# Kernel optimization log

Hardware: AMD Instinct MI355X
Metric: run time of the kernel (lower is better)

Reference implementation:

```python
import jax, jax.numpy as jnp
import numpy as np

M1, M2 = 16, 16  # Fourier modes per dim


def conv1x1(x, w, b):
    # x: [B,Ci,H,W], w: [Co,Ci], b: [Co]
    return jnp.einsum('bihw,oi->bohw', x, w) + b[None, :, None, None]


def fno_block(x, wr, wi, bw, bb):
    # x: [B,C,H,W]; wr/wi: [C,C,M1,M2]; bw: [C,C]; bb: [C]
    H, W = x.shape[-2], x.shape[-1]
    x_fft = jnp.fft.rfftn(x, axes=(-2, -1), norm='ortho')[:, :, :M1, :M2]
    w = (wr + 1j * wi).astype(jnp.complex64)
    out_fft = jnp.einsum('bikl,iokl->bokl', x_fft, w)
    # irfftn with s zero-pads truncated modes back to full spatial size
    x_spec = jnp.fft.irfftn(out_fft, s=(H, W), axes=(-2, -1), norm='ortho')
    return jax.nn.gelu(x_spec + conv1x1(x, bw, bb), approximate=False)


def setup_inputs() -> dict:
    key = jax.random.key(0)
    ks = jax.random.split(key, 8)
    B, in_c, H, W = 4, 3, 256, 256
    out_c, n_blocks, width = 4, 4, 32
    scale = 1.0 / (width * width)
    return {
        'x': jax.random.normal(ks[0], (B, in_c, H, W), jnp.float32),
        'lift_w': jax.random.normal(ks[1], (width, in_c), jnp.float32) * 0.1,
        'lift_b': jnp.zeros((width,), jnp.float32),
        'wr': jax.random.normal(ks[2], (out_c, n_blocks, width, width, M1, M2), jnp.float32) * scale,
        'wi': jax.random.normal(ks[3], (out_c, n_blocks, width, width, M1, M2), jnp.float32) * scale,
        'byp_w': jax.random.normal(ks[4], (out_c, n_blocks, width, width), jnp.float32) * 0.1,
        'byp_b': jnp.zeros((out_c, n_blocks, width), jnp.float32),
        'proj_w': jax.random.normal(ks[5], (1, width), jnp.float32) * 0.1,
        'proj_b': jnp.zeros((1,), jnp.float32),
    }


def reference(x, lift_w, lift_b, wr, wi, byp_w, byp_b, proj_w, proj_b):
    out_c, n_blocks = wr.shape[0], wr.shape[1]
    x0 = conv1x1(x, lift_w, lift_b)
    outputs = []
    for o in range(out_c):
        xb = x0
        for n in range(n_blocks):
            xb = fno_block(xb, wr[o, n], wi[o, n], byp_w[o, n], byp_b[o, n])
        outputs.append(conv1x1(xb, proj_w, proj_b))
    return jnp.concatenate(outputs, axis=1)
```

## Files before the change

### kernel.cpp

```cpp
#include <hip/hip_runtime.h>

#define NB 4
#define NC 32
#define NH 256
#define NW 256
#define NM 16
constexpr int NPIX = NH * NW;
constexpr int NP = NB * NC * NPIX;
constexpr int ZG = NB * NC * NM * NM * 2;

typedef short bf16x8 __attribute__((ext_vector_type(8)));
typedef float f32x4  __attribute__((ext_vector_type(4)));
typedef unsigned short u16;

#define MFMA16(a, b, c) __builtin_amdgcn_mfma_f32_16x16x32_bf16(a, b, c, 0, 0, 0)

__device__ __forceinline__ u16 f2bf(float f) {
    unsigned u = __float_as_uint(f);
    u += 0x7FFFu + ((u >> 16) & 1u);
    return (u16)(u >> 16);
}
__device__ __forceinline__ float bf2f(u16 h) {
    return __uint_as_float(((unsigned)h) << 16);
}

__device__ __forceinline__ float gelu_fast(float v) {
    const float ax = fabsf(v) * 0.70710678118654752f;
    const float t = __builtin_amdgcn_rcpf(1.0f + 0.3275911f * ax);
    const float y = t * (0.254829592f + t * (-0.284496736f + t * (1.421413741f +
                    t * (-1.453152027f + t * 1.061405429f))));
    const float e = __expf(-ax * ax);
    float er = 1.0f - y * e;
    er = copysignf(er, v);
    return 0.5f * v * (1.0f + er);
}

__global__ __launch_bounds__(256) void cw_prep(u16* __restrict__ cwhi, u16* __restrict__ cwlo) {
    const int id = blockIdx.x * 256 + threadIdx.x;
    const int nn = id >> 5, k = id & 31;
    const int m = ((k & 15) * nn) & 255;
    float s, c;
    sincospif((float)m * (2.0f / 256.0f), &s, &c);
    const float v = (k < 16) ? c : s;
    const u16 hi = f2bf(v);
    cwhi[id] = hi;
    cwlo[id] = f2bf(v - bf2f(hi));
}

__global__ __launch_bounds__(256) void eb_prep(u16* __restrict__ ebhi, u16* __restrict__ eblo) {
    const int id = blockIdx.x * 256 + threadIdx.x;
    const int row = id >> 8, w = id & 255;
    const int m = ((row & 15) * w) & 255;
    float s, c;
    sincospif((float)m * (2.0f / 256.0f), &s, &c);
    const float v = 0.0625f * ((row < 16) ? c : s);
    const u16 hi = f2bf(v);
    ebhi[id] = hi;
    eblo[id] = f2bf(v - bf2f(hi));
}

template<bool LIFT>
__global__ __launch_bounds__(512) void fwd_kernel(
    const float* __restrict__ src,
    const float* __restrict__ lift_w,
    const float* __restrict__ lift_b,
    const u16* __restrict__ ebhi,
    const u16* __restrict__ eblo,
    float* __restrict__ zred)
{
    __shared__ u16 Yhi[32 * 260], Ylo[32 * 260];
    __shared__ float P[32][33];

    const int tid = threadIdx.x;
    const int c  = blockIdx.x;
    const int gb = blockIdx.y;
    const int b  = gb & 3;
    const int wv = tid >> 6, lane = tid & 63;
    const int mrow = lane & 15, q = lane >> 4;

    float lw0 = 0.f, lw1 = 0.f, lw2 = 0.f, lb = 0.f;
    const float* sb;
    if (LIFT) {
        lw0 = lift_w[c * 3 + 0]; lw1 = lift_w[c * 3 + 1]; lw2 = lift_w[c * 3 + 2];
        lb = lift_b[c];
        sb = src + (size_t)b * 3 * NPIX;
    } else {
        sb = src + ((size_t)gb * NC + c) * NPIX;
    }

    f32x4 acc[2][2] = {};
    for (int ks = 0; ks < 8; ++ks) {
        bf16x8 bh[2], bl[2];
        #pragma unroll
        for (int nt = 0; nt < 2; ++nt) {
            const int off = (nt * 16 + mrow) * 256 + ks * 32 + q * 8;
            bh[nt] = *(const bf16x8*)(ebhi + off);
            bl[nt] = *(const bf16x8*)(eblo + off);
        }
        #pragma unroll
        for (int mt = 0; mt < 2; ++mt) {
            const int h = wv * 32 + mt * 16 + mrow;
            const float* xp = sb + (size_t)h * NW + ks * 32 + q * 8;
            float v[8];
            if (LIFT) {
                const float4 p0a = *(const float4*)(xp);
                const float4 p0b = *(const float4*)(xp + 4);
                const float4 p1a = *(const float4*)(xp + NPIX);
                const float4 p1b = *(const float4*)(xp + NPIX + 4);
                const float4 p2a = *(const float4*)(xp + 2 * NPIX);
                const float4 p2b = *(const float4*)(xp + 2 * NPIX + 4);
                v[0] = lw0 * p0a.x + lw1 * p1a.x + lw2 * p2a.x + lb;
                v[1] = lw0 * p0a.y + lw1 * p1a.y + lw2 * p2a.y + lb;
                v[2] = lw0 * p0a.z + lw1 * p1a.z + lw2 * p2a.z + lb;
                v[3] = lw0 * p0a.w + lw1 * p1a.w + lw2 * p2a.w + lb;
                v[4] = lw0 * p0b.x + lw1 * p1b.x + lw2 * p2b.x + lb;
                v[5] = lw0 * p0b.y + lw1 * p1b.y + lw2 * p2b.y + lb;
                v[6] = lw0 * p0b.z + lw1 * p1b.z + lw2 * p2b.z + lb;
                v[7] = lw0 * p0b.w + lw1 * p1b.w + lw2 * p2b.w + lb;
            } else {
                const float4 pa = *(const float4*)(xp);
                const float4 pb = *(const float4*)(xp + 4);
                v[0] = pa.x; v[1] = pa.y; v[2] = pa.z; v[3] = pa.w;
                v[4] = pb.x; v[5] = pb.y; v[6] = pb.z; v[7] = pb.w;
            }
            bf16x8 xh, xl;
            #pragma unroll
            for (int j = 0; j < 8; ++j) {
                const u16 hi = f2bf(v[j]);
                xh[j] = (short)hi;
                xl[j] = (short)f2bf(v[j] - bf2f(hi));
            }
            #pragma unroll
            for (int nt = 0; nt < 2; ++nt) {
                acc[mt][nt] = MFMA16(xh, bh[nt], acc[mt][nt]);
                acc[mt][nt] = MFMA16(xh, bl[nt], acc[mt][nt]);
                acc[mt][nt] = MFMA16(xl, bh[nt], acc[mt][nt]);
            }
        }
    }

    #pragma unroll
    for (int mt = 0; mt < 2; ++mt) {
        #pragma unroll
        for (int nt = 0; nt < 2; ++nt) {
            #pragma unroll
            for (int r = 0; r < 4; ++r) {
                const int h = wv * 32 + mt * 16 + q * 4 + r;
                const int combo = nt * 16 + mrow;
                const float val = acc[mt][nt][r];
                const u16 hi = f2bf(val);
                Yhi[combo * 260 + h] = hi;
                Ylo[combo * 260 + h] = f2bf(val - bf2f(hi));
            }
        }
    }
    __syncthreads();

    if (wv < 4) {
        const int mt2 = wv >> 1, nt2 = wv & 1;
        f32x4 p = {};
        for (int ks = 0; ks < 8; ++ks) {
            const int aoff = (mt2 * 16 + mrow) * 256 + ks * 32 + q * 8;
            const bf16x8 ah = *(const bf16x8*)(ebhi + aoff);
            const bf16x8 al = *(const bf16x8*)(eblo + aoff);
            const int boff = (nt2 * 16 + mrow) * 260 + ks * 32 + q * 8;
            const bf16x8 yh = *(const bf16x8*)(Yhi + boff);
            const bf16x8 yl = *(const bf16x8*)(Ylo + boff);
            p = MFMA16(ah, yh, p);
            p = MFMA16(ah, yl, p);
            p = MFMA16(al, yh, p);
        }
        #pragma unroll
        for (int r = 0; r < 4; ++r)
            P[mt2 * 16 + q * 4 + r][nt2 * 16 + mrow] = p[r];
    }
    __syncthreads();

    if (tid < 256) {
        const int k = tid >> 4, l = tid & 15;
        const float zr = P[k][l] - P[16 + k][16 + l];
        const float zi = -(P[k][16 + l] + P[16 + k][l]);
        const int idx = (gb * NC + c) * 256 + tid;
        zred[idx * 2 + 0] = zr;
        zred[idx * 2 + 1] = zi;
    }
}

__global__ __launch_bounds__(256) void mix_kernel(
    const float* __restrict__ zred,
    float* __restrict__ zmix,
    const float* __restrict__ wr,
    const float* __restrict__ wi,
    int o0, int n, int zgmul)
{
    __shared__ float ps[4][NB][64][2];
    const int tid = threadIdx.x;
    const int oc = blockIdx.x, mq = blockIdx.y, g = blockIdx.z;
    const int o = o0 + g, zg = zgmul * g;
    const int ichunk = tid >> 6, ml = tid & 63;
    const int mode = mq * 64 + ml;

    const float* wrb = wr + (size_t)(o * 4 + n) * NC * NC * 256;
    const float* wib = wi + (size_t)(o * 4 + n) * NC * NC * 256;

    float orr[NB] = {0.f, 0.f, 0.f, 0.f};
    float oii[NB] = {0.f, 0.f, 0.f, 0.f};

    #pragma unroll
    for (int ii = 0; ii < 8; ++ii) {
        const int i = ichunk * 8 + ii;
        const float wrv = wrb[(i * NC + oc) * 256 + mode];
        const float wiv = wib[(i * NC + oc) * 256 + mode];
        #pragma unroll
        for (int b = 0; b < NB; ++b) {
            const float2 z = *(const float2*)&zred[(((zg * NB + b) * NC + i) * 256 + mode) * 2];
            orr[b] += z.x * wrv - z.y * wiv;
            oii[b] += z.x * wiv + z.y * wrv;
        }
    }
    #pragma unroll
    for (int b = 0; b < NB; ++b) {
        ps[ichunk][b][ml][0] = orr[b];
        ps[ichunk][b][ml][1] = oii[b];
    }
    __syncthreads();

    const int b2 = tid >> 6, ml2 = tid & 63;
    float re = 0.f, im = 0.f;
    #pragma unroll
    for (int ic = 0; ic < 4; ++ic) {
        re += ps[ic][b2][ml2][0];
        im += ps[ic][b2][ml2][1];
    }
    const int oidx = ((g * NB + b2) * NC + oc) * 256 + mq * 64 + ml2;
    zmix[oidx * 2 + 0] = re;
    zmix[oidx * 2 + 1] = im;
}

template<bool LIFT, bool FINAL>
__global__ __launch_bounds__(256) void inv_kernel(
    const float* __restrict__ zmix,
    const float* __restrict__ src,
    const float* __restrict__ byp_w,
    const float* __restrict__ byp_b,
    const float* __restrict__ lift_w,
    const float* __restrict__ lift_b,
    const float* __restrict__ proj_w,
    const float* __restrict__ proj_b,
    const u16* __restrict__ cwhi,
    const u16* __restrict__ cwlo,
    float* __restrict__ dst,
    int o0, int n)
{
    __shared__ float2 tw[256];
    __shared__ u16 Thi[NC * 40], Tlo[NC * 40];
    __shared__ u16 Whi[NC * 40], Wlo[NC * 40];
    __shared__ float bbl[NC];
    __shared__ float bweffs[NC * 3];

    const int tid = threadIdx.x;
    const int h = blockIdx.x;
    const int gb = blockIdx.y;
    const int g = gb >> 2, b = gb & 3;
    const int o = o0 + g;

    {
        float s, cs;
        sincospif((float)tid * (2.0f / 256.0f), &s, &cs);
        tw[tid] = make_float2(cs, s);
    }

    const float* bwp = byp_w + (size_t)(o * 4 + n) * NC * NC;
    const float* bbp = byp_b + (o * 4 + n) * NC;

    if (LIFT) {
        if (tid < 96) {
            const int oc = tid / 3, j = tid % 3;
            float s = 0.f;
            for (int ic = 0; ic < NC; ++ic) s += bwp[oc * NC + ic] * lift_w[ic * 3 + j];
            bweffs[oc * 3 + j] = s;
        } else if (tid < 128) {
            const int oc = tid - 96;
            float s = bbp[oc];
            for (int ic = 0; ic < NC; ++ic) s += bwp[oc * NC + ic] * lift_b[ic];
            bbl[oc] = s;
        }
    } else {
        if (tid < NC) bbl[tid] = bbp[tid];
    }
    __syncthreads();

    for (int idx = tid; idx < NC * NC; idx += 256) {
        const int c = idx >> 5, ic = idx & 31;
        float v;
        if (LIFT) v = (ic < 3) ? bweffs[c * 3 + ic] : 0.f;
        else      v = bwp[idx];
        const u16 hi = f2bf(v);
        Whi[c * 40 + ic] = hi;
        Wlo[c * 40 + ic] = f2bf(v - bf2f(hi));
    }

    #pragma unroll
    for (int rep = 0; rep < 2; ++rep) {
        const int it = rep * 256 + tid;
        const int c = it >> 4, l = it & 15;
        const float sl = (l == 0 ? 1.0f : 2.0f) / 256.0f;
        const float* zp = zmix + ((size_t)(gb * NC + c) * 256 + l) * 2;
        float tr = 0.f, ti = 0.f;
        int m = 0;
        #pragma unroll
        for (int k = 0; k < NM; ++k) {
            const float2 z = *(const float2*)(zp + k * 32);
            const float2 t = tw[m];
            tr += z.x * t.x - z.y * t.y;
            ti += z.x * t.y + z.y * t.x;
            m = (m + h) & 255;
        }
        tr *= sl; ti *= sl;
        if (l == 0) tr += bbl[c];
        const u16 rh = f2bf(tr);
        Thi[c * 40 + l] = rh;
        Tlo[c * 40 + l] = f2bf(tr - bf2f(rh));
        const float nti_ = -ti;
        const u16 ih = f2bf(nti_);
        Thi[c * 40 + 16 + l] = ih;
        Tlo[c * 40 + 16 + l] = f2bf(nti_ - bf2f(ih));
    }
    __syncthreads();

    const int lane = tid & 63, wv = tid >> 6;
    const int mrow = lane & 15, q = lane >> 4;

    bf16x8 aThi[2], aTlo[2], aWhi[2], aWlo[2];
    #pragma unroll
    for (int mt = 0; mt < 2; ++mt) {
        const int ro = (mt * 16 + mrow) * 40 + 8 * q;
        aThi[mt] = *(const bf16x8*)&Thi[ro];
        aTlo[mt] = *(const bf16x8*)&Tlo[ro];
        aWhi[mt] = *(const bf16x8*)&Whi[ro];
        aWlo[mt] = *(const bf16x8*)&Wlo[ro];
    }

    float pwv[8];
    float pb = 0.f;
    if (FINAL) {
        #pragma unroll
        for (int mt = 0; mt < 2; ++mt)
            #pragma unroll
            for (int i = 0; i < 4; ++i)
                pwv[mt * 4 + i] = proj_w[mt * 16 + q * 4 + i];
        pb = proj_b[0];
    }

    const float* xb = src + (LIFT ? (size_t)b * 3 * NPIX : (size_t)gb * NC * NPIX) + h * NW;
    const int KIC = LIFT ? 3 : NC;

    for (int nti = 0; nti < 4; ++nti) {
        const int nt = wv * 4 + nti;
        const int ncol = nt * 16 + mrow;

        const bf16x8 cwh = *(const bf16x8*)(cwhi + ncol * 32 + 8 * q);
        const bf16x8 cwl = *(const bf16x8*)(cwlo + ncol * 32 + 8 * q);

        bf16x8 xh, xl;
        #pragma unroll
        for (int j = 0; j < 8; ++j) {
            const int k = 8 * q + j;
            const float v = (k < KIC) ? xb[(size_t)k * NPIX + ncol] : 0.f;
            const u16 hi = f2bf(v);
            xh[j] = (short)hi;
            xl[j] = (short)f2bf(v - bf2f(hi));
        }

        float fpart = 0.f;
        #pragma unroll
        for (int mt = 0; mt < 2; ++mt) {
            f32x4 acc = {0.f, 0.f, 0.f, 0.f};
            acc = MFMA16(aThi[mt], cwh, acc);
            acc = MFMA16(aThi[mt], cwl, acc);
            acc = MFMA16(aTlo[mt], cwh, acc);
            acc = MFMA16(aWhi[mt], xh, acc);
            acc = MFMA16(aWhi[mt], xl, acc);
            acc = MFMA16(aWlo[mt], xh, acc);
            if (FINAL) {
                #pragma unroll
                for (int i = 0; i < 4; ++i)
                    fpart += gelu_fast(acc[i]) * pwv[mt * 4 + i];
            } else {
                #pragma unroll
                for (int i = 0; i < 4; ++i) {
                    const int c = mt * 16 + q * 4 + i;
                    dst[((size_t)gb * NC + c) * NPIX + h * NW + ncol] = gelu_fast(acc[i]);
                }
            }
        }
        if (FINAL) {
            fpart += __shfl_xor(fpart, 16);
            fpart += __shfl_xor(fpart, 32);
            if (q == 0) {
                dst[(((size_t)b * 4 + o) * NH + h) * NW + nt * 16 + mrow] = fpart + pb;
            }
        }
    }
}

extern "C" void kernel_launch(void* const* d_in, const int* in_sizes, int n_in,
                              void* d_out, int out_size, void* d_ws, size_t ws_size,
                              hipStream_t stream)
{
    const float* x      = (const float*)d_in[0];
    const float* lift_w = (const float*)d_in[1];
    const float* lift_b = (const float*)d_in[2];
    const float* wr     = (const float*)d_in[3];
    const float* wi     = (const float*)d_in[4];
    const float* byp_w  = (const float*)d_in[5];
    const float* byp_b  = (const float*)d_in[6];
    const float* proj_w = (const float*)d_in[7];
    const float* proj_b = (const float*)d_in[8];
    float* out = (float*)d_out;
    float* ws  = (float*)d_ws;

    u16* cwhi = (u16*)ws;
    u16* cwlo = cwhi + 8192;
    u16* ebhi = cwlo + 8192;
    u16* eblo = ebhi + 8192;
    float* base = ws + 16384;

    int G = 4;
    while (G > 1) {
        const size_t need = (16384 + (size_t)2 * G * NP + (size_t)2 * G * ZG) * sizeof(float);
        if (need <= ws_size) break;
        G >>= 1;
    }

    float* bufA = base;
    float* bufB = bufA + (size_t)G * NP;
    float* zred = bufB + (size_t)G * NP;
    float* zmix = zred + (size_t)G * ZG;

    cw_prep<<<32, 256, 0, stream>>>(cwhi, cwlo);
    eb_prep<<<32, 256, 0, stream>>>(ebhi, eblo);

    for (int o0 = 0; o0 < 4; o0 += G) {
        const float* rd = nullptr;
        float* wrbuf = bufA;
        for (int n = 0; n < 4; ++n) {
            const bool lift = (n == 0);
            const bool fin  = (n == 3);
            const float* src = lift ? x : rd;

            if (lift) {
                fwd_kernel<true><<<dim3(NC, NB), 512, 0, stream>>>(src, lift_w, lift_b, ebhi, eblo, zred);
            } else {
                fwd_kernel<false><<<dim3(NC, G * NB), 512, 0, stream>>>(src, lift_w, lift_b, ebhi, eblo, zred);
            }

            mix_kernel<<<dim3(NC, 4, G), 256, 0, stream>>>(zred, zmix, wr, wi, o0, n, lift ? 0 : 1);

            dim3 igrid(NH, G * NB);
            if (fin) {
                inv_kernel<false, true><<<igrid, 256, 0, stream>>>(
                    zmix, src, byp_w, byp_b, lift_w, lift_b, proj_w, proj_b, cwhi, cwlo, out, o0, n);
            } else if (lift) {
                inv_kernel<true, false><<<igrid, 256, 0, stream>>>(
                    zmix, src, byp_w, byp_b, lift_w, lift_b, proj_w, proj_b, cwhi, cwlo, wrbuf, o0, n);
            } else {
                inv_kernel<false, false><<<igrid, 256, 0, stream>>>(
                    zmix, src, byp_w, byp_b, lift_w, lift_b, proj_w, proj_b, cwhi, cwlo, wrbuf, o0, n);
            }
            rd = wrbuf;
            wrbuf = (wrbuf == bufA) ? bufB : bufA;
        }
    }
}
```

Baseline: 547.7 us.

## Split forward DFT into two kernels for more blocks, shrink mix blocks, cap G at 2

Splits the forward truncated DFT into two kernels. The first does the W-direction transform over 64-row slabs, four blocks per channel, and writes the bf16 hi/lo intermediate to global memory. The second does the H-direction reduction. This gives four times as many blocks for the expensive first stage, at the cost of an extra launch and a global round-trip of the intermediate. It also halves mix_kernel block size to double its grid, merges the two table-prep kernels into one, and lowers the maximum group size G from 4 to 2, which doubles the number of outer passes.

```diff
diff --git a/kernel.cpp b/kernel.cpp
--- a/kernel.cpp
+++ b/kernel.cpp
@@ -35,48 +35,53 @@
     return 0.5f * v * (1.0f + er);
 }
 
-__global__ __launch_bounds__(256) void cw_prep(u16* __restrict__ cwhi, u16* __restrict__ cwlo) {
+__global__ __launch_bounds__(256) void tab_prep(
+    u16* __restrict__ cwhi, u16* __restrict__ cwlo,
+    u16* __restrict__ ebhi, u16* __restrict__ eblo)
+{
     const int id = blockIdx.x * 256 + threadIdx.x;
-    const int nn = id >> 5, k = id & 31;
-    const int m = ((k & 15) * nn) & 255;
-    float s, c;
-    sincospif((float)m * (2.0f / 256.0f), &s, &c);
-    const float v = (k < 16) ? c : s;
-    const u16 hi = f2bf(v);
-    cwhi[id] = hi;
-    cwlo[id] = f2bf(v - bf2f(hi));
-}
-
-__global__ __launch_bounds__(256) void eb_prep(u16* __restrict__ ebhi, u16* __restrict__ eblo) {
-    const int id = blockIdx.x * 256 + threadIdx.x;
-    const int row = id >> 8, w = id & 255;
-    const int m = ((row & 15) * w) & 255;
-    float s, c;
-    sincospif((float)m * (2.0f / 256.0f), &s, &c);
-    const float v = 0.0625f * ((row < 16) ? c : s);
-    const u16 hi = f2bf(v);
-    ebhi[id] = hi;
-    eblo[id] = f2bf(v - bf2f(hi));
+    if (id < 8192) {
+        const int nn = id >> 5, k = id & 31;
+        const int m = ((k & 15) * nn) & 255;
+        float s, c;
+        sincospif((float)m * (2.0f / 256.0f), &s, &c);
+        const float v = (k < 16) ? c : s;
+        const u16 hi = f2bf(v);
+        cwhi[id] = hi;
+        cwlo[id] = f2bf(v - bf2f(hi));
+    } else {
+        const int id2 = id - 8192;
+        const int row = id2 >> 8, w = id2 & 255;
+        const int m = ((row & 15) * w) & 255;
+        float s, c;
+        sincospif((float)m * (2.0f / 256.0f), &s, &c);
+        const float v = 0.0625f * ((row < 16) ? c : s);
+        const u16 hi = f2bf(v);
+        ebhi[id2] = hi;
+        eblo[id2] = f2bf(v - bf2f(hi));
+    }
 }
 
 template<bool LIFT>
-__global__ __launch_bounds__(512) void fwd_kernel(
+__global__ __launch_bounds__(256) void fwd_s1(
     const float* __restrict__ src,
     const float* __restrict__ lift_w,
     const float* __restrict__ lift_b,
     const u16* __restrict__ ebhi,
     const u16* __restrict__ eblo,
-    float* __restrict__ zred)
+    u16* __restrict__ yhi,
+    u16* __restrict__ ylo)
 {
-    __shared__ u16 Yhi[32 * 260], Ylo[32 * 260];
-    __shared__ float P[32][33];
+    __shared__ u16 TrHi[64][34], TrLo[64][34];
 
     const int tid = threadIdx.x;
     const int c  = blockIdx.x;
     const int gb = blockIdx.y;
+    const int hq = blockIdx.z;
     const int b  = gb & 3;
     const int wv = tid >> 6, lane = tid & 63;
     const int mrow = lane & 15, q = lane >> 4;
+    const int hbase = hq * 64 + wv * 16;
 
     float lw0 = 0.f, lw1 = 0.f, lw2 = 0.f, lb = 0.f;
     const float* sb;
@@ -88,7 +93,7 @@
         sb = src + ((size_t)gb * NC + c) * NPIX;
     }
 
-    f32x4 acc[2][2] = {};
+    f32x4 acc[2] = {};
     for (int ks = 0; ks < 8; ++ks) {
         bf16x8 bh[2], bl[2];
         #pragma unroll
@@ -97,108 +102,126 @@
             bh[nt] = *(const bf16x8*)(ebhi + off);
             bl[nt] = *(const bf16x8*)(eblo + off);
         }
-        #pragma unroll
-        for (int mt = 0; mt < 2; ++mt) {
-            const int h = wv * 32 + mt * 16 + mrow;
-            const float* xp = sb + (size_t)h * NW + ks * 32 + q * 8;
-            float v[8];
-            if (LIFT) {
-                const float4 p0a = *(const float4*)(xp);
-                const float4 p0b = *(const float4*)(xp + 4);
-                const float4 p1a = *(const float4*)(xp + NPIX);
-                const float4 p1b = *(const float4*)(xp + NPIX + 4);
-                const float4 p2a = *(const float4*)(xp + 2 * NPIX);
-                const float4 p2b = *(const float4*)(xp + 2 * NPIX + 4);
-                v[0] = lw0 * p0a.x + lw1 * p1a.x + lw2 * p2a.x + lb;
-                v[1] = lw0 * p0a.y + lw1 * p1a.y + lw2 * p2a.y + lb;
-                v[2] = lw0 * p0a.z + lw1 * p1a.z + lw2 * p2a.z + lb;
-                v[3] = lw0 * p0a.w + lw1 * p1a.w + lw2 * p2a.w + lb;
-                v[4] = lw0 * p0b.x + lw1 * p1b.x + lw2 * p2b.x + lb;
-                v[5] = lw0 * p0b.y + lw1 * p1b.y + lw2 * p2b.y + lb;
-                v[6] = lw0 * p0b.z + lw1 * p1b.z + lw2 * p2b.z + lb;
-                v[7] = lw0 * p0b.w + lw1 * p1b.w + lw2 * p2b.w + lb;
-            } else {
-                const float4 pa = *(const float4*)(xp);
-                const float4 pb = *(const float4*)(xp + 4);
-                v[0] = pa.x; v[1] = pa.y; v[2] = pa.z; v[3] = pa.w;
-                v[4] = pb.x; v[5] = pb.y; v[6] = pb.z; v[7] = pb.w;
-            }
-            bf16x8 xh, xl;
-            #pragma unroll
-            for (int j = 0; j < 8; ++j) {
-                const u16 hi = f2bf(v[j]);
-                xh[j] = (short)hi;
-                xl[j] = (short)f2bf(v[j] - bf2f(hi));
-            }
-            #pragma unroll
-            for (int nt = 0; nt < 2; ++nt) {
-                acc[mt][nt] = MFMA16(xh, bh[nt], acc[mt][nt]);
-                acc[mt][nt] = MFMA16(xh, bl[nt], acc[mt][nt]);
-                acc[mt][nt] = MFMA16(xl, bh[nt], acc[mt][nt]);
-            }
-        }
-    }
-
-    #pragma unroll
-    for (int mt = 0; mt < 2; ++mt) {
+        const float* xp = sb + (size_t)(hbase + mrow) * NW + ks * 32 + q * 8;
+        float v[8];
+        if (LIFT) {
+            const float4 p0a = *(const float4*)(xp);
+            const float4 p0b = *(const float4*)(xp + 4);
+            const float4 p1a = *(const float4*)(xp + NPIX);
+            const float4 p1b = *(const float4*)(xp + NPIX + 4);
+            const float4 p2a = *(const float4*)(xp + 2 * NPIX);
+            const float4 p2b = *(const float4*)(xp + 2 * NPIX + 4);
+            v[0] = lw0 * p0a.x + lw1 * p1a.x + lw2 * p2a.x + lb;
+            v[1] = lw0 * p0a.y + lw1 * p1a.y + lw2 * p2a.y + lb;
+            v[2] = lw0 * p0a.z + lw1 * p1a.z + lw2 * p2a.z + lb;
+            v[3] = lw0 * p0a.w + lw1 * p1a.w + lw2 * p2a.w + lb;
+            v[4] = lw0 * p0b.x + lw1 * p1b.x + lw2 * p2b.x + lb;
+            v[5] = lw0 * p0b.y + lw1 * p1b.y + lw2 * p2b.y + lb;
+            v[6] = lw0 * p0b.z + lw1 * p1b.z + lw2 * p2b.z + lb;
+            v[7] = lw0 * p0b.w + lw1 * p1b.w + lw2 * p2b.w + lb;
+        } else {
+            const float4 pa = *(const float4*)(xp);
+            const float4 pb = *(const float4*)(xp + 4);
+            v[0] = pa.x; v[1] = pa.y; v[2] = pa.z; v[3] = pa.w;
+            v[4] = pb.x; v[5] = pb.y; v[6] = pb.z; v[7] = pb.w;
+        }
+        bf16x8 xh, xl;
+        #pragma unroll
+        for (int j = 0; j < 8; ++j) {
+            const u16 hi = f2bf(v[j]);
+            xh[j] = (short)hi;
+            xl[j] = (short)f2bf(v[j] - bf2f(hi));
+        }
         #pragma unroll
         for (int nt = 0; nt < 2; ++nt) {
-            #pragma unroll
-            for (int r = 0; r < 4; ++r) {
-                const int h = wv * 32 + mt * 16 + q * 4 + r;
-                const int combo = nt * 16 + mrow;
-                const float val = acc[mt][nt][r];
-                const u16 hi = f2bf(val);
-                Yhi[combo * 260 + h] = hi;
-                Ylo[combo * 260 + h] = f2bf(val - bf2f(hi));
-            }
+            acc[nt] = MFMA16(xh, bh[nt], acc[nt]);
+            acc[nt] = MFMA16(xh, bl[nt], acc[nt]);
+            acc[nt] = MFMA16(xl, bh[nt], acc[nt]);
+        }
+    }
+
+    #pragma unroll
+    for (int nt = 0; nt < 2; ++nt) {
+        #pragma unroll
+        for (int r = 0; r < 4; ++r) {
+            const int hl = wv * 16 + q * 4 + r;
+            const int combo = nt * 16 + mrow;
+            const float val = acc[nt][r];
+            const u16 hi = f2bf(val);
+            TrHi[hl][combo] = hi;
+            TrLo[hl][combo] = f2bf(val - bf2f(hi));
         }
     }
     __syncthreads();
 
-    if (wv < 4) {
-        const int mt2 = wv >> 1, nt2 = wv & 1;
-        f32x4 p = {};
-        for (int ks = 0; ks < 8; ++ks) {
-            const int aoff = (mt2 * 16 + mrow) * 256 + ks * 32 + q * 8;
-            const bf16x8 ah = *(const bf16x8*)(ebhi + aoff);
-            const bf16x8 al = *(const bf16x8*)(eblo + aoff);
-            const int boff = (nt2 * 16 + mrow) * 260 + ks * 32 + q * 8;
-            const bf16x8 yh = *(const bf16x8*)(Yhi + boff);
-            const bf16x8 yl = *(const bf16x8*)(Ylo + boff);
-            p = MFMA16(ah, yh, p);
-            p = MFMA16(ah, yl, p);
-            p = MFMA16(al, yh, p);
-        }
-        #pragma unroll
-        for (int r = 0; r < 4; ++r)
-            P[mt2 * 16 + q * 4 + r][nt2 * 16 + mrow] = p[r];
-    }
+    {
+        const int combo = tid >> 3, jj = tid & 7;
+        bf16x8 vh, vl;
+        #pragma unroll
+        for (int i = 0; i < 8; ++i) {
+            vh[i] = (short)TrHi[jj * 8 + i][combo];
+            vl[i] = (short)TrLo[jj * 8 + i][combo];
+        }
+        const size_t off = (((size_t)gb * NC + c) * 32 + combo) * 256 + hq * 64 + jj * 8;
+        *(bf16x8*)(yhi + off) = vh;
+        *(bf16x8*)(ylo + off) = vl;
+    }
+}
+
+__global__ __launch_bounds__(256) void fwd_s2(
+    const u16* __restrict__ yhi,
+    const u16* __restrict__ ylo,
+    const u16* __restrict__ ebhi,
+    const u16* __restrict__ eblo,
+    float* __restrict__ zred)
+{
+    __shared__ float P[32][33];
+
+    const int tid = threadIdx.x;
+    const int c  = blockIdx.x;
+    const int gb = blockIdx.y;
+    const int wv = tid >> 6, lane = tid & 63;
+    const int mrow = lane & 15, q = lane >> 4;
+    const int mt2 = wv >> 1, nt2 = wv & 1;
+
+    f32x4 p = {};
+    const size_t ybase = (((size_t)gb * NC + c) * 32 + nt2 * 16 + mrow) * 256;
+    for (int ks = 0; ks < 8; ++ks) {
+        const int aoff = (mt2 * 16 + mrow) * 256 + ks * 32 + q * 8;
+        const bf16x8 ah = *(const bf16x8*)(ebhi + aoff);
+        const bf16x8 al = *(const bf16x8*)(eblo + aoff);
+        const bf16x8 yh = *(const bf16x8*)(yhi + ybase + ks * 32 + q * 8);
+        const bf16x8 yl = *(const bf16x8*)(ylo + ybase + ks * 32 + q * 8);
+        p = MFMA16(ah, yh, p);
+        p = MFMA16(ah, yl, p);
+        p = MFMA16(al, yh, p);
+    }
+    #pragma unroll
+    for (int r = 0; r < 4; ++r)
+        P[mt2 * 16 + q * 4 + r][nt2 * 16 + mrow] = p[r];
     __syncthreads();
 
-    if (tid < 256) {
-        const int k = tid >> 4, l = tid & 15;
-        const float zr = P[k][l] - P[16 + k][16 + l];
-        const float zi = -(P[k][16 + l] + P[16 + k][l]);
-        const int idx = (gb * NC + c) * 256 + tid;
-        zred[idx * 2 + 0] = zr;
-        zred[idx * 2 + 1] = zi;
-    }
-}
-
-__global__ __launch_bounds__(256) void mix_kernel(
+    const int k = tid >> 4, l = tid & 15;
+    const float zr = P[k][l] - P[16 + k][16 + l];
+    const float zi = -(P[k][16 + l] + P[16 + k][l]);
+    const int idx = (gb * NC + c) * 256 + tid;
+    zred[idx * 2 + 0] = zr;
+    zred[idx * 2 + 1] = zi;
+}
+
+__global__ __launch_bounds__(128) void mix_kernel(
     const float* __restrict__ zred,
     float* __restrict__ zmix,
     const float* __restrict__ wr,
     const float* __restrict__ wi,
     int o0, int n, int zgmul)
 {
-    __shared__ float ps[4][NB][64][2];
+    __shared__ float ps[4][NB][32][2];
     const int tid = threadIdx.x;
-    const int oc = blockIdx.x, mq = blockIdx.y, g = blockIdx.z;
+    const int oc = blockIdx.x, mo = blockIdx.y, g = blockIdx.z;
     const int o = o0 + g, zg = zgmul * g;
-    const int ichunk = tid >> 6, ml = tid & 63;
-    const int mode = mq * 64 + ml;
+    const int ichunk = tid >> 5, ml = tid & 31;
+    const int mode = mo * 32 + ml;
 
     const float* wrb = wr + (size_t)(o * 4 + n) * NC * NC * 256;
     const float* wib = wi + (size_t)(o * 4 + n) * NC * NC * 256;
@@ -225,14 +248,14 @@
     }
     __syncthreads();
 
-    const int b2 = tid >> 6, ml2 = tid & 63;
+    const int b2 = tid >> 5, ml2 = tid & 31;
     float re = 0.f, im = 0.f;
     #pragma unroll
     for (int ic = 0; ic < 4; ++ic) {
         re += ps[ic][b2][ml2][0];
         im += ps[ic][b2][ml2][1];
     }
-    const int oidx = ((g * NB + b2) * NC + oc) * 256 + mq * 64 + ml2;
+    const int oidx = ((g * NB + b2) * NC + oc) * 256 + mo * 32 + ml2;
     zmix[oidx * 2 + 0] = re;
     zmix[oidx * 2 + 1] = im;
 }
@@ -426,20 +449,23 @@
     u16* eblo = ebhi + 8192;
     float* base = ws + 16384;
 
-    int G = 4;
+    int G = 2;
     while (G > 1) {
-        const size_t need = (16384 + (size_t)2 * G * NP + (size_t)2 * G * ZG) * sizeof(float);
+        const size_t yfl = ((size_t)G * NB * NC * 32 * 256 * 2 * 2) / 4;
+        const size_t need = (16384 + yfl + (size_t)2 * G * NP + (size_t)2 * G * ZG) * sizeof(float);
         if (need <= ws_size) break;
         G >>= 1;
     }
 
-    float* bufA = base;
+    const size_t ycnt = (size_t)G * NB * NC * 32 * 256;
+    u16* yhi = (u16*)base;
+    u16* ylo = yhi + ycnt;
+    float* bufA = base + (ycnt * 2 * 2) / 4;
     float* bufB = bufA + (size_t)G * NP;
     float* zred = bufB + (size_t)G * NP;
     float* zmix = zred + (size_t)G * ZG;
 
-    cw_prep<<<32, 256, 0, stream>>>(cwhi, cwlo);
-    eb_prep<<<32, 256, 0, stream>>>(ebhi, eblo);
+    tab_prep<<<64, 256, 0, stream>>>(cwhi, cwlo, ebhi, eblo);
 
     for (int o0 = 0; o0 < 4; o0 += G) {
         const float* rd = nullptr;
@@ -448,14 +474,14 @@
             const bool lift = (n == 0);
             const bool fin  = (n == 3);
             const float* src = lift ? x : rd;
-
-            if (lift) {
-                fwd_kernel<true><<<dim3(NC, NB), 512, 0, stream>>>(src, lift_w, lift_b, ebhi, eblo, zred);
-            } else {
-                fwd_kernel<false><<<dim3(NC, G * NB), 512, 0, stream>>>(src, lift_w, lift_b, ebhi, eblo, zred);
-            }
-
-            mix_kernel<<<dim3(NC, 4, G), 256, 0, stream>>>(zred, zmix, wr, wi, o0, n, lift ? 0 : 1);
+            const int ngb = lift ? NB : G * NB;
+
+            if (lift) fwd_s1<true><<<dim3(NC, ngb, 4), 256, 0, stream>>>(src, lift_w, lift_b, ebhi, eblo, yhi, ylo);
+            else      fwd_s1<false><<<dim3(NC, ngb, 4), 256, 0, stream>>>(src, lift_w, lift_b, ebhi, eblo, yhi, ylo);
+
+            fwd_s2<<<dim3(NC, ngb), 256, 0, stream>>>(yhi, ylo, ebhi, eblo, zred);
+
+            mix_kernel<<<dim3(NC, 8, G), 128, 0, stream>>>(zred, zmix, wr, wi, o0, n, lift ? 0 : 1);
 
             dim3 igrid(NH, G * NB);
             if (fin) {
```

Result: slower. 602.4 us (+10.0%).

## Store intermediates as pre-split bf16 hi/lo pairs and hoist lift forward pass

Applied to the files above, without the earlier changes.

Intermediate activations are now written as packed 32-bit words holding the bf16 hi and lo halves, so later forward and inverse kernels skip the float-to-bf16 split and only repack bits. The lifted-input forward transform is computed once into its own buffer and reused across all output groups, and the two table-prep kernels are merged into one. The group count is capped at 2, trading parallelism per launch for a smaller workspace. Storage size per element is unchanged, so the saving comes from conversion arithmetic and one fewer launch rather than memory traffic.

```diff
diff --git a/kernel.cpp b/kernel.cpp
--- a/kernel.cpp
+++ b/kernel.cpp
@@ -12,6 +12,7 @@
 typedef short bf16x8 __attribute__((ext_vector_type(8)));
 typedef float f32x4  __attribute__((ext_vector_type(4)));
 typedef unsigned short u16;
+typedef unsigned int u32;
 
 #define MFMA16(a, b, c) __builtin_amdgcn_mfma_f32_16x16x32_bf16(a, b, c, 0, 0, 0)
 
@@ -22,6 +23,11 @@
 }
 __device__ __forceinline__ float bf2f(u16 h) {
     return __uint_as_float(((unsigned)h) << 16);
+}
+__device__ __forceinline__ u32 packsplit(float f) {
+    const u16 hi = f2bf(f);
+    const u16 lo = f2bf(f - bf2f(hi));
+    return (u32)hi | ((u32)lo << 16);
 }
 
 __device__ __forceinline__ float gelu_fast(float v) {
@@ -35,33 +41,36 @@
     return 0.5f * v * (1.0f + er);
 }
 
-__global__ __launch_bounds__(256) void cw_prep(u16* __restrict__ cwhi, u16* __restrict__ cwlo) {
+__global__ __launch_bounds__(256) void tab_prep(
+    u16* __restrict__ cwhi, u16* __restrict__ cwlo,
+    u16* __restrict__ ebhi, u16* __restrict__ eblo)
+{
     const int id = blockIdx.x * 256 + threadIdx.x;
-    const int nn = id >> 5, k = id & 31;
-    const int m = ((k & 15) * nn) & 255;
-    float s, c;
-    sincospif((float)m * (2.0f / 256.0f), &s, &c);
-    const float v = (k < 16) ? c : s;
-    const u16 hi = f2bf(v);
-    cwhi[id] = hi;
-    cwlo[id] = f2bf(v - bf2f(hi));
-}
-
-__global__ __launch_bounds__(256) void eb_prep(u16* __restrict__ ebhi, u16* __restrict__ eblo) {
-    const int id = blockIdx.x * 256 + threadIdx.x;
-    const int row = id >> 8, w = id & 255;
-    const int m = ((row & 15) * w) & 255;
-    float s, c;
-    sincospif((float)m * (2.0f / 256.0f), &s, &c);
-    const float v = 0.0625f * ((row < 16) ? c : s);
-    const u16 hi = f2bf(v);
-    ebhi[id] = hi;
-    eblo[id] = f2bf(v - bf2f(hi));
+    if (id < 8192) {
+        const int nn = id >> 5, k = id & 31;
+        const int m = ((k & 15) * nn) & 255;
+        float s, c;
+        sincospif((float)m * (2.0f / 256.0f), &s, &c);
+        const float v = (k < 16) ? c : s;
+        const u16 hi = f2bf(v);
+        cwhi[id] = hi;
+        cwlo[id] = f2bf(v - bf2f(hi));
+    } else {
+        const int id2 = id - 8192;
+        const int row = id2 >> 8, w = id2 & 255;
+        const int m = ((row & 15) * w) & 255;
+        float s, c;
+        sincospif((float)m * (2.0f / 256.0f), &s, &c);
+        const float v = 0.0625f * ((row < 16) ? c : s);
+        const u16 hi = f2bf(v);
+        ebhi[id2] = hi;
+        eblo[id2] = f2bf(v - bf2f(hi));
+    }
 }
 
 template<bool LIFT>
 __global__ __launch_bounds__(512) void fwd_kernel(
-    const float* __restrict__ src,
+    const void* __restrict__ srcv,
     const float* __restrict__ lift_w,
     const float* __restrict__ lift_b,
     const u16* __restrict__ ebhi,
@@ -79,13 +88,14 @@
     const int mrow = lane & 15, q = lane >> 4;
 
     float lw0 = 0.f, lw1 = 0.f, lw2 = 0.f, lb = 0.f;
-    const float* sb;
+    const float* sbf = nullptr;
+    const u32* sbp = nullptr;
     if (LIFT) {
         lw0 = lift_w[c * 3 + 0]; lw1 = lift_w[c * 3 + 1]; lw2 = lift_w[c * 3 + 2];
         lb = lift_b[c];
-        sb = src + (size_t)b * 3 * NPIX;
+        sbf = (const float*)srcv + (size_t)b * 3 * NPIX;
     } else {
-        sb = src + ((size_t)gb * NC + c) * NPIX;
+        sbp = (const u32*)srcv + ((size_t)gb * NC + c) * NPIX;
     }
 
     f32x4 acc[2][2] = {};
@@ -100,15 +110,16 @@
         #pragma unroll
         for (int mt = 0; mt < 2; ++mt) {
             const int h = wv * 32 + mt * 16 + mrow;
-            const float* xp = sb + (size_t)h * NW + ks * 32 + q * 8;
-            float v[8];
+            bf16x8 xh, xl;
             if (LIFT) {
+                const float* xp = sbf + (size_t)h * NW + ks * 32 + q * 8;
                 const float4 p0a = *(const float4*)(xp);
                 const float4 p0b = *(const float4*)(xp + 4);
                 const float4 p1a = *(const float4*)(xp + NPIX);
                 const float4 p1b = *(const float4*)(xp + NPIX + 4);
                 const float4 p2a = *(const float4*)(xp + 2 * NPIX);
                 const float4 p2b = *(const float4*)(xp + 2 * NPIX + 4);
+                float v[8];
                 v[0] = lw0 * p0a.x + lw1 * p1a.x + lw2 * p2a.x + lb;
                 v[1] = lw0 * p0a.y + lw1 * p1a.y + lw2 * p2a.y + lb;
                 v[2] = lw0 * p0a.z + lw1 * p1a.z + lw2 * p2a.z + lb;
@@ -117,18 +128,27 @@
                 v[5] = lw0 * p0b.y + lw1 * p1b.y + lw2 * p2b.y + lb;
                 v[6] = lw0 * p0b.z + lw1 * p1b.z + lw2 * p2b.z + lb;
                 v[7] = lw0 * p0b.w + lw1 * p1b.w + lw2 * p2b.w + lb;
+                #pragma unroll
+                for (int j = 0; j < 8; ++j) {
+                    const u16 hi = f2bf(v[j]);
+                    xh[j] = (short)hi;
+                    xl[j] = (short)f2bf(v[j] - bf2f(hi));
+                }
             } else {
-                const float4 pa = *(const float4*)(xp);
-                const float4 pb = *(const float4*)(xp + 4);
-                v[0] = pa.x; v[1] = pa.y; v[2] = pa.z; v[3] = pa.w;
-                v[4] = pb.x; v[5] = pb.y; v[6] = pb.z; v[7] = pb.w;
-            }
-            bf16x8 xh, xl;
-            #pragma unroll
-            for (int j = 0; j < 8; ++j) {
-                const u16 hi = f2bf(v[j]);
-                xh[j] = (short)hi;
-                xl[j] = (short)f2bf(v[j] - bf2f(hi));
+                const u32* xp = sbp + (size_t)h * NW + ks * 32 + q * 8;
+                const uint4 pa = *(const uint4*)(xp);
+                const uint4 pb = *(const uint4*)(xp + 4);
+                u32 p[8] = {pa.x, pa.y, pa.z, pa.w, pb.x, pb.y, pb.z, pb.w};
+                union { uint4 u; bf16x8 v; } ch, cl;
+                ch.u.x = (p[0] & 0xFFFFu) | (p[1] << 16);
+                ch.u.y = (p[2] & 0xFFFFu) | (p[3] << 16);
+                ch.u.z = (p[4] & 0xFFFFu) | (p[5] << 16);
+                ch.u.w = (p[6] & 0xFFFFu) | (p[7] << 16);
+                cl.u.x = (p[0] >> 16) | (p[1] & 0xFFFF0000u);
+                cl.u.y = (p[2] >> 16) | (p[3] & 0xFFFF0000u);
+                cl.u.z = (p[4] >> 16) | (p[5] & 0xFFFF0000u);
+                cl.u.w = (p[6] >> 16) | (p[7] & 0xFFFF0000u);
+                xh = ch.v; xl = cl.v;
             }
             #pragma unroll
             for (int nt = 0; nt < 2; ++nt) {
@@ -240,7 +260,7 @@
 template<bool LIFT, bool FINAL>
 __global__ __launch_bounds__(256) void inv_kernel(
     const float* __restrict__ zmix,
-    const float* __restrict__ src,
+    const void* __restrict__ srcv,
     const float* __restrict__ byp_w,
     const float* __restrict__ byp_b,
     const float* __restrict__ lift_w,
@@ -249,7 +269,7 @@
     const float* __restrict__ proj_b,
     const u16* __restrict__ cwhi,
     const u16* __restrict__ cwlo,
-    float* __restrict__ dst,
+    void* __restrict__ dstv,
     int o0, int n)
 {
     __shared__ float2 tw[256];
@@ -352,8 +372,10 @@
         pb = proj_b[0];
     }
 
-    const float* xb = src + (LIFT ? (size_t)b * 3 * NPIX : (size_t)gb * NC * NPIX) + h * NW;
-    const int KIC = LIFT ? 3 : NC;
+    const float* xbf = LIFT ? (const float*)srcv + (size_t)b * 3 * NPIX + h * NW : nullptr;
+    const u32*   xbp = LIFT ? nullptr : (const u32*)srcv + (size_t)gb * NC * NPIX + h * NW;
+    u32*   dstp = (u32*)dstv;
+    float* dstf = (float*)dstv;
 
     for (int nti = 0; nti < 4; ++nti) {
         const int nt = wv * 4 + nti;
@@ -366,10 +388,16 @@
         #pragma unroll
         for (int j = 0; j < 8; ++j) {
             const int k = 8 * q + j;
-            const float v = (k < KIC) ? xb[(size_t)k * NPIX + ncol] : 0.f;
-            const u16 hi = f2bf(v);
-            xh[j] = (short)hi;
-            xl[j] = (short)f2bf(v - bf2f(hi));
+            if (LIFT) {
+                const float v = (k < 3) ? xbf[(size_t)k * NPIX + ncol] : 0.f;
+                const u16 hi = f2bf(v);
+                xh[j] = (short)hi;
+                xl[j] = (short)f2bf(v - bf2f(hi));
+            } else {
+                const u32 p = xbp[(size_t)k * NPIX + ncol];
+                xh[j] = (short)(p & 0xFFFFu);
+                xl[j] = (short)(p >> 16);
+            }
         }
 
         float fpart = 0.f;
@@ -390,7 +418,7 @@
                 #pragma unroll
                 for (int i = 0; i < 4; ++i) {
                     const int c = mt * 16 + q * 4 + i;
-                    dst[((size_t)gb * NC + c) * NPIX + h * NW + ncol] = gelu_fast(acc[i]);
+                    dstp[((size_t)gb * NC + c) * NPIX + h * NW + ncol] = packsplit(gelu_fast(acc[i]));
                 }
             }
         }
@@ -398,7 +426,7 @@
             fpart += __shfl_xor(fpart, 16);
             fpart += __shfl_xor(fpart, 32);
             if (q == 0) {
-                dst[(((size_t)b * 4 + o) * NH + h) * NW + nt * 16 + mrow] = fpart + pb;
+                dstf[(((size_t)b * 4 + o) * NH + h) * NW + nt * 16 + mrow] = fpart + pb;
             }
         }
     }
@@ -417,7 +445,6 @@
     const float* byp_b  = (const float*)d_in[6];
     const float* proj_w = (const float*)d_in[7];
     const float* proj_b = (const float*)d_in[8];
-    float* out = (float*)d_out;
     float* ws  = (float*)d_ws;
 
     u16* cwhi = (u16*)ws;
@@ -426,47 +453,46 @@
     u16* eblo = ebhi + 8192;
     float* base = ws + 16384;
 
-    int G = 4;
+    int G = 2;
     while (G > 1) {
-        const size_t need = (16384 + (size_t)2 * G * NP + (size_t)2 * G * ZG) * sizeof(float);
+        const size_t need = (16384 + 65536 + (size_t)2 * G * ZG + (size_t)2 * G * NP) * sizeof(float);
         if (need <= ws_size) break;
         G >>= 1;
     }
 
-    float* bufA = base;
-    float* bufB = bufA + (size_t)G * NP;
-    float* zred = bufB + (size_t)G * NP;
-    float* zmix = zred + (size_t)G * ZG;
-
-    cw_prep<<<32, 256, 0, stream>>>(cwhi, cwlo);
-    eb_prep<<<32, 256, 0, stream>>>(ebhi, eblo);
+    float* zlift = base;
+    float* zred  = zlift + 65536;
+    float* zmix  = zred + (size_t)G * ZG;
+    u32* bufA = (u32*)(zmix + (size_t)G * ZG);
+    u32* bufB = bufA + (size_t)G * NP;
+
+    tab_prep<<<64, 256, 0, stream>>>(cwhi, cwlo, ebhi, eblo);
+
+    fwd_kernel<true><<<dim3(NC, NB), 512, 0, stream>>>(x, lift_w, lift_b, ebhi, eblo, zlift);
 
     for (int o0 = 0; o0 < 4; o0 += G) {
-        const float* rd = nullptr;
-        float* wrbuf = bufA;
+        const u32* rd = nullptr;
+        u32* wrbuf = bufA;
         for (int n = 0; n < 4; ++n) {
             const bool lift = (n == 0);
             const bool fin  = (n == 3);
-            const float* src = lift ? x : rd;
-
-            if (lift) {
-                fwd_kernel<true><<<dim3(NC, NB), 512, 0, stream>>>(src, lift_w, lift_b, ebhi, eblo, zred);
-            } else {
-                fwd_kernel<false><<<dim3(NC, G * NB), 512, 0, stream>>>(src, lift_w, lift_b, ebhi, eblo, zred);
-            }
-
-            mix_kernel<<<dim3(NC, 4, G), 256, 0, stream>>>(zred, zmix, wr, wi, o0, n, lift ? 0 : 1);
+
+            if (!lift)
+                fwd_kernel<false><<<dim3(NC, G * NB), 512, 0, stream>>>(rd, lift_w, lift_b, ebhi, eblo, zred);
+
+            mix_kernel<<<dim3(NC, 4, G), 256, 0, stream>>>(
+                lift ? zlift : zred, zmix, wr, wi, o0, n, lift ? 0 : 1);
 
             dim3 igrid(NH, G * NB);
             if (fin) {
                 inv_kernel<false, true><<<igrid, 256, 0, stream>>>(
-                    zmix, src, byp_w, byp_b, lift_w, lift_b, proj_w, proj_b, cwhi, cwlo, out, o0, n);
+                    zmix, rd, byp_w, byp_b, lift_w, lift_b, proj_w, proj_b, cwhi, cwlo, d_out, o0, n);
             } else if (lift) {
                 inv_kernel<true, false><<<igrid, 256, 0, stream>>>(
-                    zmix, src, byp_w, byp_b, lift_w, lift_b, proj_w, proj_b, cwhi, cwlo, wrbuf, o0, n);
+                    zmix, x, byp_w, byp_b, lift_w, lift_b, proj_w, proj_b, cwhi, cwlo, wrbuf, o0, n);
             } else {
                 inv_kernel<false, false><<<igrid, 256, 0, stream>>>(
-                    zmix, src, byp_w, byp_b, lift_w, lift_b, proj_w, proj_b, cwhi, cwlo, wrbuf, o0, n);
+                    zmix, rd, byp_w, byp_b, lift_w, lift_b, proj_w, proj_b, cwhi, cwlo, wrbuf, o0, n);
             }
             rd = wrbuf;
             wrbuf = (wrbuf == bufA) ? bufB : bufA;
```

Result: faster. 531.0 us (-3.0%).
